# Performance work log

Measured on AMD Instinct MI355X. Metric: run time of the kernel, lower is better.

## Reference

```python
import jax, jax.numpy as jnp
import numpy as np

E = 8      # num_experts
K = 2      # top-k
DIM = 1024
DFF = 2048  # fused gate+up width; intermediate = DFF // 2 == DIM


def setup_inputs() -> dict:
    key = jax.random.key(0)
    ks = jax.random.split(key, 5)
    B, S = 4, 2048
    x = jax.random.normal(ks[0], (B, S, DIM), dtype=jnp.float32)
    Wg = jax.random.normal(ks[1], (E, DIM), dtype=jnp.float32) * 0.02
    bg = jax.random.normal(ks[2], (E,), dtype=jnp.float32) * 0.02
    w1 = jax.random.normal(ks[3], (E, DFF, DIM), dtype=jnp.float32) * 0.02
    w2 = jax.random.normal(ks[4], (E, DIM, DFF // 2), dtype=jnp.float32) * 0.02
    return {"x": x, "Wg": Wg, "bg": bg, "w1": w1, "w2": w2}


def _moe(x, Wg, bg, w1, w2):
    B, S, D = x.shape
    t = x.reshape(-1, D)                      # [T, D] tokens
    logits = t @ Wg.T + bg                    # [T, E]
    probs = jax.nn.softmax(logits, axis=-1)
    topw, topi = jax.lax.top_k(probs, K)      # [T, K]
    topw = topw / jnp.sum(topw, axis=-1, keepdims=True)  # renormalize=True
    # per-token combine weight for each expert (0 if not selected): [T, E]
    combine = jnp.sum(jax.nn.one_hot(topi, E, dtype=t.dtype) * topw[..., None], axis=1)

    def body(acc, packed):
        w1e, w2e, ce = packed                 # [DFF, D], [D, DFF//2], [T]
        h = t @ w1e.T                         # [T, DFF]
        gate, up = jnp.split(h, 2, axis=-1)   # silu_and_mul (SwiGLU)
        a = jax.nn.silu(gate) * up            # [T, DFF//2]
        o = a @ w2e.T                         # [T, D]
        return acc + ce[:, None] * o, None

    out, _ = jax.lax.scan(body, jnp.zeros_like(t), (w1, w2, combine.T))
    return out.reshape(B, S, D)


def reference(x, Wg, bg, w1, w2):
    return _moe(x, Wg, bg, w1, w2)
```

## Files before the change

kernel.cpp:

```cpp
#include <hip/hip_runtime.h>
#include <hip/hip_bf16.h>
#include <cstdint>

#define T_TOKENS 8192
#define DIM 1024
#define NEXP 8
#define DFFH 1024
#define ROWCAP 17408
#define NCHUNK 16

typedef __attribute__((ext_vector_type(8))) short bf16x8;
typedef __attribute__((ext_vector_type(4))) float f32x4;

__device__ __forceinline__ ushort f2bf(float f) {
  uint32_t u = __float_as_uint(f);
  uint32_t r = (u + 0x7fffu + ((u >> 16) & 1u)) >> 16;
  return (ushort)r;
}

__device__ __forceinline__ void async16(const void* g, const void* l) {
  __builtin_amdgcn_global_load_lds(
      (const __attribute__((address_space(1))) void*)(uintptr_t)g,
      (__attribute__((address_space(3))) void*)(uintptr_t)l, 16, 0, 0);
}

__global__ __launch_bounds__(256) void cast_kernel(
    const float4* __restrict__ x, const float4* __restrict__ w1,
    const float4* __restrict__ w2, ushort* __restrict__ xb,
    ushort* __restrict__ w1b, ushort* __restrict__ w2b) {
  const int NX = T_TOKENS * DIM / 4;
  const int NW1 = NEXP * 2048 * DIM / 4;
  const int NW2 = NEXP * DIM * DFFH / 4;
  const int total = NX + NW1 + NW2;
  for (int i = blockIdx.x * 256 + threadIdx.x; i < total; i += 2048 * 256) {
    float4 v; ushort* dst;
    if (i < NX) { v = x[i]; dst = xb + (size_t)i * 4; }
    else if (i < NX + NW1) { int j = i - NX; v = w1[j]; dst = w1b + (size_t)j * 4; }
    else { int j = i - NX - NW1; v = w2[j]; dst = w2b + (size_t)j * 4; }
    ushort4 o4;
    o4.x = f2bf(v.x); o4.y = f2bf(v.y); o4.z = f2bf(v.z); o4.w = f2bf(v.w);
    *(ushort4*)dst = o4;
  }
}

__global__ __launch_bounds__(256) void gate_kernel(
    const float4* __restrict__ x4, const float4* __restrict__ Wg4,
    const float* __restrict__ bg, int* __restrict__ top2e,
    float2* __restrict__ top2w) {
  __shared__ float4 wgl[NEXP * 256];
  const int tid = threadIdx.x;
  for (int i = tid; i < NEXP * 256; i += 256) wgl[i] = Wg4[i];
  __syncthreads();
  const int wave = tid >> 6, lane = tid & 63;
  const float bgsel = bg[lane & 7];
  const int t0 = (blockIdx.x * 4 + wave) * 16;
  for (int tt = 0; tt < 16; ++tt) {
    const int t = t0 + tt;
    const float4* xr = x4 + (size_t)t * 256;
    float acc[NEXP];
#pragma unroll
    for (int e = 0; e < NEXP; ++e) acc[e] = 0.f;
#pragma unroll
    for (int j = 0; j < 4; ++j) {
      float4 xv = xr[lane + j * 64];
#pragma unroll
      for (int e = 0; e < NEXP; ++e) {
        float4 wv = wgl[e * 256 + lane + j * 64];
        acc[e] += xv.x * wv.x + xv.y * wv.y + xv.z * wv.z + xv.w * wv.w;
      }
    }
#pragma unroll
    for (int e = 0; e < NEXP; ++e) {
      float v = acc[e];
      v += __shfl_xor(v, 1); v += __shfl_xor(v, 2); v += __shfl_xor(v, 4);
      acc[e] = v;
    }
    float v = acc[0];
#pragma unroll
    for (int e = 1; e < NEXP; ++e) v = ((lane & 7) == e) ? acc[e] : v;
    v += __shfl_xor(v, 8); v += __shfl_xor(v, 16); v += __shfl_xor(v, 32);
    v += bgsel;
    float m1 = v;
    m1 = fmaxf(m1, __shfl_xor(m1, 1));
    m1 = fmaxf(m1, __shfl_xor(m1, 2));
    m1 = fmaxf(m1, __shfl_xor(m1, 4));
    unsigned long long mk = __ballot(v == m1);
    int bi = (int)(__ffsll(mk) - 1) & 7;
    float v2 = (((lane & 7) == bi) ? -1e30f : v);
    float m2 = v2;
    m2 = fmaxf(m2, __shfl_xor(m2, 1));
    m2 = fmaxf(m2, __shfl_xor(m2, 2));
    m2 = fmaxf(m2, __shfl_xor(m2, 4));
    mk = __ballot(v2 == m2);
    int si = (int)(__ffsll(mk) - 1) & 7;
    if (lane == 0) {
      float w0 = 1.f / (1.f + __expf(m2 - m1));
      top2e[t] = bi | (si << 8);
      top2w[t] = make_float2(w0, 1.f - w0);
    }
  }
}

__global__ __launch_bounds__(1024) void route_kernel(
    const int* __restrict__ top2e, int* __restrict__ cnt,
    int* __restrict__ off, int* __restrict__ base ) {
  __shared__ int chunkcnt[NCHUNK][NEXP];
  const int tid = threadIdx.x;
  int c[NEXP];
#pragma unroll
  for (int e = 0; e < NEXP; ++e) c[e] = 0;
  const int4* p = (const int4*)(top2e + tid * 8);
  int4 a = p[0], b = p[1];
  int vals[8] = {a.x, a.y, a.z, a.w, b.x, b.y, b.z, b.w};
#pragma unroll
  for (int k = 0; k < 8; ++k) {
    int e0 = vals[k] & 255, e1 = (vals[k] >> 8) & 255;
#pragma unroll
    for (int e = 0; e < NEXP; ++e) c[e] += (e0 == e) + (e1 == e);
  }
#pragma unroll
  for (int e = 0; e < NEXP; ++e) {
    c[e] += __shfl_xor(c[e], 1);  c[e] += __shfl_xor(c[e], 2);
    c[e] += __shfl_xor(c[e], 4);  c[e] += __shfl_xor(c[e], 8);
    c[e] += __shfl_xor(c[e], 16); c[e] += __shfl_xor(c[e], 32);
  }
  const int wave = tid >> 6, lane = tid & 63;
  if (lane == 0) {
#pragma unroll
    for (int e = 0; e < NEXP; ++e) chunkcnt[wave][e] = c[e];
  }
  __syncthreads();
  if (tid == 0) {
    int o = 0;
    off[0] = 0;
    for (int e = 0; e < NEXP; ++e) {
      int tot = 0;
      for (int w = 0; w < NCHUNK; ++w) tot += chunkcnt[w][e];
      cnt[e] = tot;
      int run = o;
      for (int w = 0; w < NCHUNK; ++w) { base[w * NEXP + e] = run; run += chunkcnt[w][e]; }
      o += (tot + 127) & ~127;
      off[e + 1] = o;
    }
  }
}

__global__ __launch_bounds__(512) void scatter_kernel(
    const int* __restrict__ top2e, const float2* __restrict__ top2w,
    const int* __restrict__ base, int* __restrict__ rows_token,
    float* __restrict__ rows_weight) {
  __shared__ int lcnt[NEXP];
  const int tid = threadIdx.x;
  if (tid < NEXP) lcnt[tid] = 0;
  __syncthreads();
  const int b = blockIdx.x;
  const int t = b * 512 + tid;
  int pk = top2e[t];
  float2 w = top2w[t];
  int e0 = pk & 255, e1 = (pk >> 8) & 255;
  int p0 = atomicAdd(&lcnt[e0], 1);
  int p1 = atomicAdd(&lcnt[e1], 1);
  int r0 = base[b * NEXP + e0] + p0;
  int r1 = base[b * NEXP + e1] + p1;
  rows_token[r0] = t; rows_weight[r0] = w.x;
  rows_token[r1] = t; rows_weight[r1] = w.y;
}

__global__ __launch_bounds__(256) void mlpA_kernel(
    const ushort* __restrict__ xb, const ushort* __restrict__ w1b,
    const int* __restrict__ rows_token, const int* __restrict__ cnt,
    const int* __restrict__ off, ushort* __restrict__ abuf) {
  const int e = blockIdx.z, mt = blockIdx.y, nt = blockIdx.x;
  const int count = cnt[e];
  if (mt * 128 >= count) return;
  const int base = off[e];

  __shared__ ushort As[2][128 * 64];
  __shared__ ushort Bs[2][2][64 * 64];

  const int tid = threadIdx.x;
  const int wave = tid >> 6, lane = tid & 63;
  const int wm = wave >> 1, wn = wave & 1;
  const int cg = tid & 7;
  const int r7w = (tid >> 3) & 7;
  const int cgs = (cg ^ r7w) * 8;

  const ushort* gA[4];
#pragma unroll
  for (int i = 0; i < 4; ++i) {
    int row = i * 32 + (tid >> 3);
    int r = mt * 128 + row;
    int tok = (r < count) ? rows_token[base + r] : 0;
    gA[i] = xb + ((size_t)tok * DIM + cgs);
  }
  const ushort* gBg[2];
  const ushort* gBu[2];
#pragma unroll
  for (int i = 0; i < 2; ++i) {
    int row = i * 32 + (tid >> 3);
    gBg[i] = w1b + ((size_t)(e * 2048 + nt * 64 + row) * DIM + cgs);
    gBu[i] = w1b + ((size_t)(e * 2048 + 1024 + nt * 64 + row) * DIM + cgs);
  }

#define STAGE_A1(b_, k0_)                                             \
  {                                                                   \
    _Pragma("unroll")                                                 \
    for (int i = 0; i < 4; ++i)                                       \
      async16(gA[i] + (k0_), &As[b_][(i * 256 + wave * 64) * 8]);     \
    _Pragma("unroll")                                                 \
    for (int i = 0; i < 2; ++i) {                                     \
      async16(gBg[i] + (k0_), &Bs[b_][0][(i * 256 + wave * 64) * 8]); \
      async16(gBu[i] + (k0_), &Bs[b_][1][(i * 256 + wave * 64) * 8]); \
    }                                                                 \
  }

  const f32x4 zero = {0.f, 0.f, 0.f, 0.f};
  f32x4 accg[4][2], accu[4][2];
#pragma unroll
  for (int m = 0; m < 4; ++m)
#pragma unroll
    for (int n = 0; n < 2; ++n) { accg[m][n] = zero; accu[m][n] = zero; }

  const int xr = (lane & 7) << 3;

  STAGE_A1(0, 0);
  __syncthreads();

  for (int t = 0; t < 16; ++t) {
    const int b = t & 1;
    if (t < 15) STAGE_A1(b ^ 1, (t + 1) * 64);
#pragma unroll
    for (int kk = 0; kk < 2; ++kk) {
      const int ko = (kk * 32 + (lane >> 4) * 8) ^ xr;
      bf16x8 af[4];
#pragma unroll
      for (int m = 0; m < 4; ++m)
        af[m] = *(const bf16x8*)&As[b][(wm * 64 + m * 16 + (lane & 15)) * 64 + ko];
#pragma unroll
      for (int n = 0; n < 2; ++n) {
        bf16x8 bgf = *(const bf16x8*)&Bs[b][0][(wn * 32 + n * 16 + (lane & 15)) * 64 + ko];
        bf16x8 buf_ = *(const bf16x8*)&Bs[b][1][(wn * 32 + n * 16 + (lane & 15)) * 64 + ko];
#pragma unroll
        for (int m = 0; m < 4; ++m) {
          accg[m][n] = __builtin_amdgcn_mfma_f32_16x16x32_bf16(af[m], bgf, accg[m][n], 0, 0, 0);
          accu[m][n] = __builtin_amdgcn_mfma_f32_16x16x32_bf16(af[m], buf_, accu[m][n], 0, 0, 0);
        }
      }
    }
    __syncthreads();
  }

  const size_t arow0 = (size_t)(base + mt * 128 + wm * 64);
#pragma unroll
  for (int m = 0; m < 4; ++m)
#pragma unroll
    for (int n = 0; n < 2; ++n)
#pragma unroll
      for (int r = 0; r < 4; ++r) {
        float g = accg[m][n][r], u = accu[m][n][r];
        float a = (g / (1.f + __expf(-g))) * u;
        size_t row = arow0 + m * 16 + (lane >> 4) * 4 + r;
        int col = nt * 64 + wn * 32 + n * 16 + (lane & 15);
        abuf[row * DFFH + col] = f2bf(a);
      }
}

__global__ __launch_bounds__(256) void mlpB_kernel(
    const ushort* __restrict__ abuf, const ushort* __restrict__ w2b,
    const int* __restrict__ rows_token, const float* __restrict__ rows_weight,
    const int* __restrict__ cnt, const int* __restrict__ off,
    float* __restrict__ out) {
  const int e = blockIdx.z, mt = blockIdx.y, nt = blockIdx.x;
  const int count = cnt[e];
  if (mt * 128 >= count) return;
  const int base = off[e];

  __shared__ ushort As[2][128 * 64];
  __shared__ ushort Bs[2][128 * 64];

  const int tid = threadIdx.x;
  const int wave = tid >> 6, lane = tid & 63;
  const int wm = wave >> 1, wn = wave & 1;
  const int cg = tid & 7;
  const int r7w = (tid >> 3) & 7;
  const int cgs = (cg ^ r7w) * 8;

  const ushort* gA[4];
#pragma unroll
  for (int i = 0; i < 4; ++i) {
    int row = i * 32 + (tid >> 3);
    gA[i] = abuf + ((size_t)(base + mt * 128 + row) * DFFH + cgs);
  }
  const ushort* gB[4];
#pragma unroll
  for (int i = 0; i < 4; ++i) {
    int row = i * 32 + (tid >> 3);
    gB[i] = w2b + ((size_t)(e * 1024 + nt * 128 + row) * DFFH + cgs);
  }

#define STAGE_B1(b_, k0_)                                           \
  {                                                                 \
    _Pragma("unroll")                                               \
    for (int i = 0; i < 4; ++i) {                                   \
      async16(gA[i] + (k0_), &As[b_][(i * 256 + wave * 64) * 8]);   \
      async16(gB[i] + (k0_), &Bs[b_][(i * 256 + wave * 64) * 8]);   \
    }                                                               \
  }

  const f32x4 zero = {0.f, 0.f, 0.f, 0.f};
  f32x4 acc[4][4];
#pragma unroll
  for (int m = 0; m < 4; ++m)
#pragma unroll
    for (int n = 0; n < 4; ++n) acc[m][n] = zero;

  const int xr = (lane & 7) << 3;

  STAGE_B1(0, 0);
  __syncthreads();

  for (int t = 0; t < 16; ++t) {
    const int b = t & 1;
    if (t < 15) STAGE_B1(b ^ 1, (t + 1) * 64);
#pragma unroll
    for (int kk = 0; kk < 2; ++kk) {
      const int ko = (kk * 32 + (lane >> 4) * 8) ^ xr;
      bf16x8 af[4];
#pragma unroll
      for (int m = 0; m < 4; ++m)
        af[m] = *(const bf16x8*)&As[b][(wm * 64 + m * 16 + (lane & 15)) * 64 + ko];
#pragma unroll
      for (int n = 0; n < 4; ++n) {
        bf16x8 bf_ = *(const bf16x8*)&Bs[b][(wn * 64 + n * 16 + (lane & 15)) * 64 + ko];
#pragma unroll
        for (int m = 0; m < 4; ++m)
          acc[m][n] = __builtin_amdgcn_mfma_f32_16x16x32_bf16(af[m], bf_, acc[m][n], 0, 0, 0);
      }
    }
    __syncthreads();
  }

#pragma unroll
  for (int m = 0; m < 4; ++m) {
#pragma unroll
    for (int r = 0; r < 4; ++r) {
      int lrow = mt * 128 + wm * 64 + m * 16 + (lane >> 4) * 4 + r;
      if (lrow < count) {
        int tok = rows_token[base + lrow];
        float wgt = rows_weight[base + lrow];
#pragma unroll
        for (int n = 0; n < 4; ++n) {
          atomicAdd(&out[(size_t)tok * DIM + nt * 128 + wn * 64 + n * 16 + (lane & 15)],
                    wgt * acc[m][n][r]);
        }
      }
    }
  }
}

extern "C" void kernel_launch(void* const* d_in, const int* in_sizes, int n_in,
                              void* d_out, int out_size, void* d_ws, size_t ws_size,
                              hipStream_t stream) {
  const float* x = (const float*)d_in[0];
  const float* Wg = (const float*)d_in[1];
  const float* bg = (const float*)d_in[2];
  const float* w1 = (const float*)d_in[3];
  const float* w2 = (const float*)d_in[4];
  float* out = (float*)d_out;

  char* ws = (char*)d_ws;
  ushort* xb = (ushort*)ws;
  ushort* w1b = xb + (size_t)T_TOKENS * DIM;
  ushort* w2b = w1b + (size_t)NEXP * 2048 * DIM;
  ushort* abuf = w2b + (size_t)NEXP * DIM * DFFH;
  char* p = (char*)(abuf + (size_t)ROWCAP * DFFH);
  int* top2e = (int*)p;            p += T_TOKENS * 4;
  float2* top2w = (float2*)p;      p += T_TOKENS * 8;
  int* rows_token = (int*)p;       p += ROWCAP * 4;
  float* rows_weight = (float*)p;  p += ROWCAP * 4;
  int* cnt = (int*)p;              p += 32;
  int* off = (int*)p;              p += 64;
  int* base = (int*)p;             p += NCHUNK * NEXP * 4;

  hipMemsetAsync(out, 0, (size_t)out_size * sizeof(float), stream);

  cast_kernel<<<2048, 256, 0, stream>>>((const float4*)x, (const float4*)w1,
                                        (const float4*)w2, xb, w1b, w2b);
  gate_kernel<<<128, 256, 0, stream>>>((const float4*)x, (const float4*)Wg, bg,
                                       top2e, top2w);
  route_kernel<<<1, 1024, 0, stream>>>(top2e, cnt, off, base);
  scatter_kernel<<<NCHUNK, 512, 0, stream>>>(top2e, top2w, base, rows_token,
                                             rows_weight);
  mlpA_kernel<<<dim3(16, 64, 8), 256, 0, stream>>>(xb, w1b, rows_token, cnt, off, abuf);
  mlpB_kernel<<<dim3(8, 64, 8), 256, 0, stream>>>(abuf, w2b, rows_token, rows_weight,
                                                  cnt, off, out);
}
```

Baseline: 262.2 us.

## Replace atomic scatter-add with bf16 row buffer and per-token combine kernel

The second GEMM no longer does float atomicAdd into the output. It writes weighted bf16 rows into a buffer that reuses the xb workspace. A new combine kernel sums each token's two expert rows through a token-to-row map recorded during scatter, which also removes the output memset. The mlpB tile is narrowed to 64 columns, and both GEMMs use a flattened 1D grid ordered so blocks sharing the same N tile run together. The intermediate bf16 rounding adds precision loss, and reusing xb as obuf depends on mlpA having finished with it.

```diff
diff --git a/kernel.cpp b/kernel.cpp
--- a/kernel.cpp
+++ b/kernel.cpp
@@ -16,6 +16,9 @@
   uint32_t u = __float_as_uint(f);
   uint32_t r = (u + 0x7fffu + ((u >> 16) & 1u)) >> 16;
   return (ushort)r;
+}
+__device__ __forceinline__ float bf2f(ushort u) {
+  return __uint_as_float(((uint32_t)u) << 16);
 }
 
 __device__ __forceinline__ void async16(const void* g, const void* l) {
@@ -148,7 +151,7 @@
 __global__ __launch_bounds__(512) void scatter_kernel(
     const int* __restrict__ top2e, const float2* __restrict__ top2w,
     const int* __restrict__ base, int* __restrict__ rows_token,
-    float* __restrict__ rows_weight) {
+    float* __restrict__ rows_weight, int2* __restrict__ tok2row) {
   __shared__ int lcnt[NEXP];
   const int tid = threadIdx.x;
   if (tid < NEXP) lcnt[tid] = 0;
@@ -164,13 +167,17 @@
   int r1 = base[b * NEXP + e1] + p1;
   rows_token[r0] = t; rows_weight[r0] = w.x;
   rows_token[r1] = t; rows_weight[r1] = w.y;
+  tok2row[t] = make_int2(r0, r1);
 }
 
 __global__ __launch_bounds__(256) void mlpA_kernel(
     const ushort* __restrict__ xb, const ushort* __restrict__ w1b,
     const int* __restrict__ rows_token, const int* __restrict__ cnt,
     const int* __restrict__ off, ushort* __restrict__ abuf) {
-  const int e = blockIdx.z, mt = blockIdx.y, nt = blockIdx.x;
+  const int bid = blockIdx.x;
+  const int nt = bid >> 9;
+  const int gidx = bid & 511;
+  const int mt = gidx & 63, e = gidx >> 6;
   const int count = cnt[e];
   if (mt * 128 >= count) return;
   const int base = off[e];
@@ -267,16 +274,18 @@
 
 __global__ __launch_bounds__(256) void mlpB_kernel(
     const ushort* __restrict__ abuf, const ushort* __restrict__ w2b,
-    const int* __restrict__ rows_token, const float* __restrict__ rows_weight,
-    const int* __restrict__ cnt, const int* __restrict__ off,
-    float* __restrict__ out) {
-  const int e = blockIdx.z, mt = blockIdx.y, nt = blockIdx.x;
+    const float* __restrict__ rows_weight, const int* __restrict__ cnt,
+    const int* __restrict__ off, ushort* __restrict__ obuf) {
+  const int bid = blockIdx.x;
+  const int nt = bid >> 9;
+  const int gidx = bid & 511;
+  const int mt = gidx & 63, e = gidx >> 6;
   const int count = cnt[e];
   if (mt * 128 >= count) return;
   const int base = off[e];
 
   __shared__ ushort As[2][128 * 64];
-  __shared__ ushort Bs[2][128 * 64];
+  __shared__ ushort Bs[2][64 * 64];
 
   const int tid = threadIdx.x;
   const int wave = tid >> 6, lane = tid & 63;
@@ -291,28 +300,29 @@
     int row = i * 32 + (tid >> 3);
     gA[i] = abuf + ((size_t)(base + mt * 128 + row) * DFFH + cgs);
   }
-  const ushort* gB[4];
-#pragma unroll
-  for (int i = 0; i < 4; ++i) {
+  const ushort* gB[2];
+#pragma unroll
+  for (int i = 0; i < 2; ++i) {
     int row = i * 32 + (tid >> 3);
-    gB[i] = w2b + ((size_t)(e * 1024 + nt * 128 + row) * DFFH + cgs);
+    gB[i] = w2b + ((size_t)(e * 1024 + nt * 64 + row) * DFFH + cgs);
   }
 
 #define STAGE_B1(b_, k0_)                                           \
   {                                                                 \
     _Pragma("unroll")                                               \
-    for (int i = 0; i < 4; ++i) {                                   \
+    for (int i = 0; i < 4; ++i)                                     \
       async16(gA[i] + (k0_), &As[b_][(i * 256 + wave * 64) * 8]);   \
+    _Pragma("unroll")                                               \
+    for (int i = 0; i < 2; ++i)                                     \
       async16(gB[i] + (k0_), &Bs[b_][(i * 256 + wave * 64) * 8]);   \
-    }                                                               \
   }
 
   const f32x4 zero = {0.f, 0.f, 0.f, 0.f};
-  f32x4 acc[4][4];
+  f32x4 acc[4][2];
 #pragma unroll
   for (int m = 0; m < 4; ++m)
 #pragma unroll
-    for (int n = 0; n < 4; ++n) acc[m][n] = zero;
+    for (int n = 0; n < 2; ++n) acc[m][n] = zero;
 
   const int xr = (lane & 7) << 3;
 
@@ -330,8 +340,8 @@
       for (int m = 0; m < 4; ++m)
         af[m] = *(const bf16x8*)&As[b][(wm * 64 + m * 16 + (lane & 15)) * 64 + ko];
 #pragma unroll
-      for (int n = 0; n < 4; ++n) {
-        bf16x8 bf_ = *(const bf16x8*)&Bs[b][(wn * 64 + n * 16 + (lane & 15)) * 64 + ko];
+      for (int n = 0; n < 2; ++n) {
+        bf16x8 bf_ = *(const bf16x8*)&Bs[b][(wn * 32 + n * 16 + (lane & 15)) * 64 + ko];
 #pragma unroll
         for (int m = 0; m < 4; ++m)
           acc[m][n] = __builtin_amdgcn_mfma_f32_16x16x32_bf16(af[m], bf_, acc[m][n], 0, 0, 0);
@@ -346,16 +356,33 @@
     for (int r = 0; r < 4; ++r) {
       int lrow = mt * 128 + wm * 64 + m * 16 + (lane >> 4) * 4 + r;
       if (lrow < count) {
-        int tok = rows_token[base + lrow];
         float wgt = rows_weight[base + lrow];
 #pragma unroll
-        for (int n = 0; n < 4; ++n) {
-          atomicAdd(&out[(size_t)tok * DIM + nt * 128 + wn * 64 + n * 16 + (lane & 15)],
-                    wgt * acc[m][n][r]);
+        for (int n = 0; n < 2; ++n) {
+          int col = nt * 64 + wn * 32 + n * 16 + (lane & 15);
+          obuf[(size_t)(base + lrow) * DIM + col] = f2bf(wgt * acc[m][n][r]);
         }
       }
     }
   }
+}
+
+__global__ __launch_bounds__(256) void combine_kernel(
+    const ushort* __restrict__ obuf, const int2* __restrict__ tok2row,
+    float* __restrict__ out) {
+  const int t = blockIdx.x;
+  int2 rr = tok2row[t];
+  const ushort4* p0 = (const ushort4*)(obuf + (size_t)rr.x * DIM);
+  const ushort4* p1 = (const ushort4*)(obuf + (size_t)rr.y * DIM);
+  float4* po = (float4*)(out + (size_t)t * DIM);
+  const int c = threadIdx.x;
+  ushort4 a = p0[c], b = p1[c];
+  float4 o;
+  o.x = bf2f(a.x) + bf2f(b.x);
+  o.y = bf2f(a.y) + bf2f(b.y);
+  o.z = bf2f(a.z) + bf2f(b.z);
+  o.w = bf2f(a.w) + bf2f(b.w);
+  po[c] = o;
 }
 
 extern "C" void kernel_launch(void* const* d_in, const int* in_sizes, int n_in,
@@ -378,11 +405,11 @@
   float2* top2w = (float2*)p;      p += T_TOKENS * 8;
   int* rows_token = (int*)p;       p += ROWCAP * 4;
   float* rows_weight = (float*)p;  p += ROWCAP * 4;
+  int2* tok2row = (int2*)p;        p += T_TOKENS * 8;
   int* cnt = (int*)p;              p += 32;
   int* off = (int*)p;              p += 64;
   int* base = (int*)p;             p += NCHUNK * NEXP * 4;
-
-  hipMemsetAsync(out, 0, (size_t)out_size * sizeof(float), stream);
+  ushort* obuf = xb;
 
   cast_kernel<<<2048, 256, 0, stream>>>((const float4*)x, (const float4*)w1,
                                         (const float4*)w2, xb, w1b, w2b);
@@ -390,8 +417,8 @@
                                        top2e, top2w);
   route_kernel<<<1, 1024, 0, stream>>>(top2e, cnt, off, base);
   scatter_kernel<<<NCHUNK, 512, 0, stream>>>(top2e, top2w, base, rows_token,
-                                             rows_weight);
-  mlpA_kernel<<<dim3(16, 64, 8), 256, 0, stream>>>(xb, w1b, rows_token, cnt, off, abuf);
-  mlpB_kernel<<<dim3(8, 64, 8), 256, 0, stream>>>(abuf, w2b, rows_token, rows_weight,
-                                                  cnt, off, out);
-}
+                                             rows_weight, tok2row);
+  mlpA_kernel<<<16 * 512, 256, 0, stream>>>(xb, w1b, rows_token, cnt, off, abuf);
+  mlpB_kernel<<<16 * 512, 256, 0, stream>>>(abuf, w2b, rows_weight, cnt, off, obuf);
+  combine_kernel<<<T_TOKENS, 256, 0, stream>>>(obuf, tok2row, out);
+}
```

New measurement: 311.7 us. 18.9% more time.
